# Kernel tuning notes

Measured on AMD Instinct MI355X. Metric: run time of the kernel, lower is better.

## Reference

```python
import jax, jax.numpy as jnp
import numpy as np

DIM = 1024
N_HEADS = 16
HEAD_DIM = DIM // N_HEADS  # 64
FF_DIM = 4096
BATCH = 2
SEQ = 2048
EPS = 1e-8
ROPE_BASE = 10000.0


def _rope_cos_sin(seq_len, head_dim):
    # inv_freq: [head_dim//2]
    inv_freq = 1.0 / (ROPE_BASE ** (jnp.arange(0, head_dim, 2, dtype=jnp.float32) / head_dim))
    t = jnp.arange(seq_len, dtype=jnp.float32)
    freqs = jnp.einsum('i,j->ij', t, inv_freq)          # [S, D/2]
    emb = jnp.concatenate([freqs, freqs], axis=-1)       # [S, D]
    return jnp.cos(emb), jnp.sin(emb)


def _apply_rope(x, cos, sin):
    # x: [B, S, H, D]; cos/sin: [S, D] -> broadcast [1, S, 1, D]
    d2 = x.shape[-1] // 2
    x1, x2 = x[..., :d2], x[..., d2:]
    cos = cos[None, :, None, :]
    sin = sin[None, :, None, :]
    cos1, cos2 = cos[..., :d2], cos[..., d2:]
    sin1, sin2 = sin[..., :d2], sin[..., d2:]
    return jnp.concatenate([x1 * cos1 - x2 * sin1, x1 * sin2 + x2 * cos2], axis=-1)


def _rmsnorm(x, scale):
    # norm = ||x||_2 * d^{-1/2}; out = scale * x / (norm + eps)
    norm = jnp.sqrt(jnp.sum(x * x, axis=-1, keepdims=True)) * (x.shape[-1] ** -0.5)
    return scale * x / (norm + EPS)


def setup_inputs() -> dict:
    key = jax.random.key(0)
    ks = jax.random.split(key, 10)
    s = lambda fan_in: 1.0 / np.sqrt(fan_in)
    return {
        'x': jax.random.normal(ks[0], (BATCH, SEQ, DIM), dtype=jnp.float32),
        'w_qkv': jax.random.normal(ks[1], (DIM, 3 * DIM), dtype=jnp.float32) * s(DIM),
        'w_attn_out': jax.random.normal(ks[2], (DIM, DIM), dtype=jnp.float32) * s(DIM),
        'w_gate': jax.random.normal(ks[3], (DIM, FF_DIM), dtype=jnp.float32) * s(DIM),
        'b_gate': jax.random.normal(ks[4], (FF_DIM,), dtype=jnp.float32) * 0.01,
        'w_lin': jax.random.normal(ks[5], (DIM, FF_DIM), dtype=jnp.float32) * s(DIM),
        'b_lin': jax.random.normal(ks[6], (FF_DIM,), dtype=jnp.float32) * 0.01,
        'w_ff_out': jax.random.normal(ks[7], (FF_DIM, DIM), dtype=jnp.float32) * s(FF_DIM),
        'scale1': jnp.ones((DIM,), dtype=jnp.float32),
        'scale2': jnp.ones((DIM,), dtype=jnp.float32),
    }


def reference(x, w_qkv, w_attn_out, w_gate, b_gate, w_lin, b_lin, w_ff_out, scale1, scale2):
    B, S, _ = x.shape
    residual = x
    qkv = (x @ w_qkv).reshape(B, S, 3, N_HEADS, HEAD_DIM)
    q, k, v = qkv[:, :, 0], qkv[:, :, 1], qkv[:, :, 2]  # [B, S, H, D]
    cos, sin = _rope_cos_sin(S, HEAD_DIM)
    q = _apply_rope(q, cos, sin)
    k = _apply_rope(k, cos, sin)
    # attention scores [B, H, S, S]
    attn = jnp.einsum('bqhd,bkhd->bhqk', q, k) / np.sqrt(HEAD_DIM).astype(np.float32)
    attn = jax.nn.softmax(attn, axis=-1)
    out = jnp.einsum('bhqk,bkhd->bqhd', attn, v).reshape(B, S, DIM)
    out = out @ w_attn_out
    x = _rmsnorm(residual + out, scale1)
    residual = x
    ff = jax.nn.sigmoid(x @ w_gate + b_gate) * (x @ w_lin + b_lin)
    ff = ff @ w_ff_out
    x = _rmsnorm(residual + ff, scale2)
    return x
```

## Files before the change

### kernel.cpp

```cpp
#include <hip/hip_runtime.h>
#include <stdint.h>

#define DIMN 1024
#define NH 16
#define HD 64
#define FFN 4096
#define BBATCH 2
#define SSEQ 2048
#define MROWS (BBATCH*SSEQ)

typedef __bf16 bf16;
typedef __bf16 bf16x8 __attribute__((ext_vector_type(8)));
typedef __bf16 bf16x4 __attribute__((ext_vector_type(4)));
typedef float f32x4 __attribute__((ext_vector_type(4)));
typedef float f32x16 __attribute__((ext_vector_type(16)));
typedef uint32_t u32x4 __attribute__((ext_vector_type(4)));

#define AS1 __attribute__((address_space(1)))
#define AS3 __attribute__((address_space(3)))

__device__ __forceinline__ void gload16(const bf16* g, bf16* l) {
  __builtin_amdgcn_global_load_lds((AS1 const void*)g, (AS3 void*)l, 16, 0, 0);
}

__device__ __forceinline__ uint32_t pkbf(float a, float b) {
  union { bf16 h[2]; uint32_t u; } x;
  x.h[0] = (bf16)a; x.h[1] = (bf16)b;
  return x.u;
}

__global__ void rope_table_kernel(float* __restrict__ tab) {
  int i = blockIdx.x * blockDim.x + threadIdx.x;
  int s = i >> 5, d = i & 31;
  float invf = exp2f(-(float)d * 0.4152410118609203f);
  float fr = (float)s * invf;
  tab[s*64 + d]      = cosf(fr);
  tab[s*64 + 32 + d] = sinf(fr);
}

__global__ void cast_f32_bf16(const float* __restrict__ in, bf16* __restrict__ out, int n4) {
  int i = blockIdx.x * blockDim.x + threadIdx.x;
  if (i < n4) {
    f32x4 v = ((const f32x4*)in)[i];
    bf16x4 o = {(bf16)v.x, (bf16)v.y, (bf16)v.z, (bf16)v.w};
    ((bf16x4*)out)[i] = o;
  }
}

__global__ __launch_bounds__(256) void transpose_cast_f32_bf16(
    const float* __restrict__ in, bf16* __restrict__ out, int R, int C) {
  __shared__ float t[32][33];
  int bx = blockIdx.x, by = blockIdx.y;
  int x = threadIdx.x, y = threadIdx.y;
  #pragma unroll
  for (int j = 0; j < 4; ++j) {
    int r = by*32 + y*4 + j;
    t[y*4+j][x] = in[(size_t)r*C + bx*32 + x];
  }
  __syncthreads();
  #pragma unroll
  for (int j = 0; j < 4; ++j) {
    int c = bx*32 + y*4 + j;
    out[(size_t)c*R + by*32 + x] = (bf16)t[x][y*4+j];
  }
}

template<int NP>
__global__ __launch_bounds__(256) void rmsnorm_sum_kernel(
    const float* __restrict__ parts, const float* __restrict__ resid,
    const float* __restrict__ sc,
    float* __restrict__ outf, bf16* __restrict__ outb) {
  int row = blockIdx.x;
  int tid = threadIdx.x;
  size_t off = (size_t)row * DIMN;
  f32x4 v = ((const f32x4*)(resid + off))[tid];
  #pragma unroll
  for (int p = 0; p < NP; ++p) {
    f32x4 a = ((const f32x4*)(parts + (size_t)p * MROWS * DIMN + off))[tid];
    v.x += a.x; v.y += a.y; v.z += a.z; v.w += a.w;
  }
  float ss = v.x*v.x + v.y*v.y + v.z*v.z + v.w*v.w;
  #pragma unroll
  for (int m = 1; m < 64; m <<= 1) ss += __shfl_xor(ss, m);
  __shared__ float red[4];
  if ((tid & 63) == 0) red[tid >> 6] = ss;
  __syncthreads();
  float tot = red[0] + red[1] + red[2] + red[3];
  float inv = 1.f / (sqrtf(tot) * 0.03125f + 1e-8f);
  f32x4 s4 = ((const f32x4*)sc)[tid];
  f32x4 o = {v.x*s4.x*inv, v.y*s4.y*inv, v.z*s4.z*inv, v.w*s4.w*inv};
  if (outf) ((f32x4*)(outf + off))[tid] = o;
  if (outb) {
    bf16x4 ob = {(bf16)o.x, (bf16)o.y, (bf16)o.z, (bf16)o.w};
    ((bf16x4*)(outb + off))[tid] = ob;
  }
}

template<int EPI>
__global__ void __launch_bounds__(256, 2) gemm_bt(
    const bf16* __restrict__ A, const bf16* __restrict__ B,
    int M, int N, int K,
    void* __restrict__ o0, void* __restrict__ o1, void* __restrict__ o2,
    const void* __restrict__ a0, const void* __restrict__ a1) {
  constexpr bool FUSED = (EPI == 5);
  __shared__ __align__(16) bf16 sh_a[2*4096];
  __shared__ __align__(16) bf16 sh_b[2*4096];
  __shared__ __align__(16) bf16 sh_c[FUSED ? 2*4096 : 4];
  const int tid  = threadIdx.x;
  const int lane = tid & 63;
  const int wid  = tid >> 6;

  int gx  = gridDim.x;
  int bid = blockIdx.y * gx + blockIdx.x;
  int nwg = gx * gridDim.y;
  int cpx = nwg >> 3;
  int swz = (bid & 7) * cpx + (bid >> 3);
  int bxi = swz % gx, byi = swz / gx;

  const int m0 = byi * 128, n0 = bxi * 128;
  const int wm = (wid >> 1) * 64, wn = (wid & 1) * 64;

  const int kb = blockIdx.z;
  const int KC = K / (int)gridDim.z;

  f32x4 acc[4][4] = {};
  f32x4 acc2[FUSED ? 4 : 1][FUSED ? 4 : 1] = {};

  const bf16* a_base = A + (size_t)m0 * K + (size_t)kb * KC;
  const bf16* b_base = B + (size_t)n0 * K + (size_t)kb * KC;
  const bf16* c_base = nullptr;
  if constexpr (FUSED) c_base = (const bf16*)o1 + (size_t)n0 * K;

  auto stage = [&](int kt, int buf) {
    const int lb = buf * 4096;
    #pragma unroll
    for (int i = 0; i < 2; ++i) {
      int idx = i*256 + tid;
      size_t go = (size_t)(idx >> 2)*K + (size_t)kt*32 + (idx & 3)*8;
      gload16(a_base + go, &sh_a[lb + idx*8]);
    }
    #pragma unroll
    for (int i = 0; i < 2; ++i) {
      int idx = i*256 + tid;
      size_t go = (size_t)(idx >> 2)*K + (size_t)kt*32 + (idx & 3)*8;
      gload16(b_base + go, &sh_b[lb + idx*8]);
    }
    if constexpr (FUSED) {
      #pragma unroll
      for (int i = 0; i < 2; ++i) {
        int idx = i*256 + tid;
        size_t go = (size_t)(idx >> 2)*K + (size_t)kt*32 + (idx & 3)*8;
        gload16(c_base + go, &sh_c[lb + idx*8]);
      }
    }
  };

  const int nsteps = KC >> 5;
  stage(0, 0);
  for (int t = 0; t < nsteps; ++t) {
    const int cb = t & 1;
    if (t + 1 < nsteps) {
      stage(t+1, cb ^ 1);
      if constexpr (FUSED) asm volatile("s_waitcnt vmcnt(6)" ::: "memory");
      else                 asm volatile("s_waitcnt vmcnt(4)" ::: "memory");
    } else {
      asm volatile("s_waitcnt vmcnt(0)" ::: "memory");
    }
    __builtin_amdgcn_sched_barrier(0);
    __builtin_amdgcn_s_barrier();
    __builtin_amdgcn_sched_barrier(0);

    const int lb = cb * 4096;
    bf16x8 af[4], bfr[4];
    #pragma unroll
    for (int m = 0; m < 4; ++m)
      af[m] = *(const bf16x8*)&sh_a[lb + (wm + m*16 + (lane & 15))*32 + (lane >> 4)*8];
    #pragma unroll
    for (int n = 0; n < 4; ++n)
      bfr[n] = *(const bf16x8*)&sh_b[lb + (wn + n*16 + (lane & 15))*32 + (lane >> 4)*8];
    __builtin_amdgcn_s_setprio(1);
    #pragma unroll
    for (int m = 0; m < 4; ++m)
      #pragma unroll
      for (int n = 0; n < 4; ++n)
        acc[m][n] = __builtin_amdgcn_mfma_f32_16x16x32_bf16(af[m], bfr[n], acc[m][n], 0, 0, 0);
    __builtin_amdgcn_s_setprio(0);
    if constexpr (FUSED) {
      bf16x8 cf[4];
      #pragma unroll
      for (int n = 0; n < 4; ++n)
        cf[n] = *(const bf16x8*)&sh_c[lb + (wn + n*16 + (lane & 15))*32 + (lane >> 4)*8];
      __builtin_amdgcn_s_setprio(1);
      #pragma unroll
      for (int m = 0; m < 4; ++m)
        #pragma unroll
        for (int n = 0; n < 4; ++n)
          acc2[m][n] = __builtin_amdgcn_mfma_f32_16x16x32_bf16(af[m], cf[n], acc2[m][n], 0, 0, 0);
      __builtin_amdgcn_s_setprio(0);
    }
    __builtin_amdgcn_sched_barrier(0);
    __builtin_amdgcn_s_barrier();
  }

  const int rq = (lane >> 4) * 4;
  const int cl = lane & 15;

  if constexpr (EPI == 0) {
    bf16* q_p = (bf16*)o0; bf16* k_p = (bf16*)o1; bf16* v_p = (bf16*)o2;
    const float* rope = (const float*)a0;
    int sec = (n0 + wn) >> 10;
    int h   = ((n0 + wn) & 1023) >> 6;
    const float qsc = (sec == 0) ? 0.18033688011112042f : 1.0f;
    #pragma unroll
    for (int m = 0; m < 4; ++m) {
      #pragma unroll
      for (int reg = 0; reg < 4; ++reg) {
        int r  = m0 + wm + m*16 + rq + reg;
        int b_ = r >> 11, s_ = r & 2047;
        int tile = s_ >> 5;
        size_t tb = ((size_t)(b_*NH + h) * 64 + tile) * 2048;
        if (sec == 2) {
          int kvl = s_ & 31;
          int ks = kvl >> 4, hiv = (kvl >> 3) & 1, jv = kvl & 7;
          #pragma unroll
          for (int n = 0; n < 4; ++n) {
            int half = n >> 1;
            int qlv  = (n & 1) * 16 + cl;
            v_p[tb + (size_t)(ks*2 + half)*512 + (hiv*32 + qlv)*8 + jv] =
                (bf16)acc[m][n][reg];
          }
        } else {
          int qlt = s_ & 31;
          bf16* dst = (sec == 0 ? q_p : k_p);
          int lo = ((cl >> 3) * 32 + qlt) * 8 + (cl & 7);
          #pragma unroll
          for (int n = 0; n < 2; ++n) {
            int d1 = n*16 + cl;
            float c1 = rope[s_*64 + d1];
            float s1 = rope[s_*64 + 32 + d1];
            float x1 = acc[m][n][reg], x2 = acc[m][n+2][reg];
            dst[tb + (size_t)n*512 + lo]       = (bf16)((x1*c1 - x2*s1) * qsc);
            dst[tb + (size_t)(n+2)*512 + lo]   = (bf16)((x1*s1 + x2*c1) * qsc);
          }
        }
      }
    }
  } else if constexpr (EPI == 1) {
    float* op = (float*)o0;
    const float* rp = (const float*)a0;
    #pragma unroll
    for (int m = 0; m < 4; ++m)
      #pragma unroll
      for (int n = 0; n < 4; ++n)
        #pragma unroll
        for (int reg = 0; reg < 4; ++reg) {
          int r = m0 + wm + m*16 + rq + reg;
          int c = n0 + wn + n*16 + cl;
          op[(size_t)r*N + c] = acc[m][n][reg] + rp[(size_t)r*N + c];
        }
  } else if constexpr (EPI == 4) {
    float* op = (float*)o0 + (size_t)kb * M * N;
    #pragma unroll
    for (int m = 0; m < 4; ++m)
      #pragma unroll
      for (int n = 0; n < 4; ++n)
        #pragma unroll
        for (int reg = 0; reg < 4; ++reg) {
          int r = m0 + wm + m*16 + rq + reg;
          int c = n0 + wn + n*16 + cl;
          op[(size_t)r*N + c] = acc[m][n][reg];
        }
  } else if constexpr (EPI == 5) {
    bf16* op = (bf16*)o0;
    const float* bg = (const float*)a0;
    const float* bl = (const float*)a1;
    #pragma unroll
    for (int m = 0; m < 4; ++m)
      #pragma unroll
      for (int n = 0; n < 4; ++n)
        #pragma unroll
        for (int reg = 0; reg < 4; ++reg) {
          int r = m0 + wm + m*16 + rq + reg;
          int c = n0 + wn + n*16 + cl;
          float gv = acc[m][n][reg] + bg[c];
          float lv = acc2[m][n][reg] + bl[c];
          float s  = 1.f / (1.f + __expf(-gv));
          op[(size_t)r*N + c] = (bf16)(s * lv);
        }
  }
}

__global__ void __launch_bounds__(256) attn_kernel(
    const bf16* __restrict__ qf_g, const bf16* __restrict__ kf_g,
    const bf16* __restrict__ vf_g, bf16* __restrict__ ao_g) {
  __shared__ __align__(16) bf16 lds_k[2*2048];
  __shared__ __align__(16) bf16 lds_v[2*2048];
  const int tid  = threadIdx.x;
  const int lane = tid & 63;
  const int qw   = tid >> 6;
  const int hi   = lane >> 5;
  const int ql   = lane & 31;
  const int bh   = blockIdx.y;
  const int b_   = bh >> 4, h = bh & 15;
  const int q0   = blockIdx.x * 128 + qw * 32;
  const int qt   = blockIdx.x * 4 + qw;

  const bf16* qtile = qf_g + ((size_t)bh*64 + qt) * 2048;
  const bf16* kbase = kf_g + (size_t)bh * 64 * 2048;
  const bf16* vbase = vf_g + (size_t)bh * 64 * 2048;

  bf16x8 qf[4];
  #pragma unroll
  for (int ds = 0; ds < 4; ++ds)
    qf[ds] = *(const bf16x8*)&qtile[ds*512 + lane*8];

  f32x16 o0 = {}, o1 = {};
  float lrun = 0.f;

  gload16(kbase + tid*8, &lds_k[tid*8]);
  gload16(vbase + tid*8, &lds_v[tid*8]);

  for (int t = 0; t < 64; ++t) {
    const int cur = (t & 1) * 2048;
    if (t < 63) {
      const int nxt = 2048 - cur;
      gload16(kbase + (size_t)(t+1)*2048 + tid*8, &lds_k[nxt + tid*8]);
      gload16(vbase + (size_t)(t+1)*2048 + tid*8, &lds_v[nxt + tid*8]);
      asm volatile("s_waitcnt vmcnt(2)" ::: "memory");
    } else {
      asm volatile("s_waitcnt vmcnt(0)" ::: "memory");
    }
    __builtin_amdgcn_sched_barrier(0);
    __builtin_amdgcn_s_barrier();
    __builtin_amdgcn_sched_barrier(0);

    f32x16 st = {};
    __builtin_amdgcn_s_setprio(1);
    #pragma unroll
    for (int ds = 0; ds < 4; ++ds) {
      bf16x8 kf = *(const bf16x8*)&lds_k[cur + ds*512 + lane*8];
      st = __builtin_amdgcn_mfma_f32_32x32x16_bf16(kf, qf[ds], st, 0, 0, 0);
    }
    __builtin_amdgcn_s_setprio(0);
    float p[16];
    float psum = 0.f;
    #pragma unroll
    for (int r = 0; r < 16; ++r) { p[r] = __builtin_amdgcn_exp2f(st[r]); psum += p[r]; }
    lrun += psum;

    uint32_t w0 = pkbf(p[0],p[1]),   w1 = pkbf(p[2],p[3]);
    uint32_t w2 = pkbf(p[4],p[5]),   w3 = pkbf(p[6],p[7]);
    uint32_t w4 = pkbf(p[8],p[9]),   w5 = pkbf(p[10],p[11]);
    uint32_t w6 = pkbf(p[12],p[13]), w7 = pkbf(p[14],p[15]);
    asm("v_permlane32_swap_b32 %0, %1" : "+v"(w0), "+v"(w2));
    asm("v_permlane32_swap_b32 %0, %1" : "+v"(w1), "+v"(w3));
    asm("v_permlane32_swap_b32 %0, %1" : "+v"(w4), "+v"(w6));
    asm("v_permlane32_swap_b32 %0, %1" : "+v"(w5), "+v"(w7));

    __builtin_amdgcn_s_setprio(1);
    {
      union { u32x4 u; bf16x8 b; } pu;
      u32x4 pwa = {w0, w1, w2, w3};
      pu.u = pwa;
      bf16x8 v0 = *(const bf16x8*)&lds_v[cur + 0*512 + lane*8];
      bf16x8 v1 = *(const bf16x8*)&lds_v[cur + 1*512 + lane*8];
      o0 = __builtin_amdgcn_mfma_f32_32x32x16_bf16(v0, pu.b, o0, 0, 0, 0);
      o1 = __builtin_amdgcn_mfma_f32_32x32x16_bf16(v1, pu.b, o1, 0, 0, 0);
      u32x4 pwb = {w4, w5, w6, w7};
      pu.u = pwb;
      bf16x8 v2 = *(const bf16x8*)&lds_v[cur + 2*512 + lane*8];
      bf16x8 v3 = *(const bf16x8*)&lds_v[cur + 3*512 + lane*8];
      o0 = __builtin_amdgcn_mfma_f32_32x32x16_bf16(v2, pu.b, o0, 0, 0, 0);
      o1 = __builtin_amdgcn_mfma_f32_32x32x16_bf16(v3, pu.b, o1, 0, 0, 0);
    }
    __builtin_amdgcn_s_setprio(0);

    __builtin_amdgcn_sched_barrier(0);
    __builtin_amdgcn_s_barrier();
    __builtin_amdgcn_sched_barrier(0);
  }

  lrun += __shfl_xor(lrun, 32);
  float inv = 1.f / lrun;
  bf16* aop = ao_g + ((size_t)(b_*SSEQ) + q0 + ql) * DIMN + h*HD;
  #pragma unroll
  for (int g = 0; g < 4; ++g) {
    int dbase = 8*g + 4*hi;
    bf16x4 w0 = {(bf16)(o0[4*g]*inv), (bf16)(o0[4*g+1]*inv),
                 (bf16)(o0[4*g+2]*inv), (bf16)(o0[4*g+3]*inv)};
    *(bf16x4*)&aop[dbase] = w0;
    bf16x4 w1 = {(bf16)(o1[4*g]*inv), (bf16)(o1[4*g+1]*inv),
                 (bf16)(o1[4*g+2]*inv), (bf16)(o1[4*g+3]*inv)};
    *(bf16x4*)&aop[32 + dbase] = w1;
  }
}

extern "C" void kernel_launch(void* const* d_in, const int* in_sizes, int n_in,
                              void* d_out, int out_size, void* d_ws, size_t ws_size,
                              hipStream_t stream) {
  const float* x      = (const float*)d_in[0];
  const float* w_qkv  = (const float*)d_in[1];
  const float* w_ao   = (const float*)d_in[2];
  const float* w_gate = (const float*)d_in[3];
  const float* b_gate = (const float*)d_in[4];
  const float* w_lin  = (const float*)d_in[5];
  const float* b_lin  = (const float*)d_in[6];
  const float* w_ffo  = (const float*)d_in[7];
  const float* scale1 = (const float*)d_in[8];
  const float* scale2 = (const float*)d_in[9];
  float* out = (float*)d_out;
  (void)ws_size; (void)in_sizes; (void)n_in; (void)out_size;

  uint8_t* ws = (uint8_t*)d_ws;
  bf16*  wt_ws   = (bf16*) (ws + 0);
  float* rope_ws = (float*)(ws + 8388608);
  bf16*  xb_ws   = (bf16*) (ws + 8912896);
  bf16*  ao_ws   = (bf16*) (ws + 8912896);
  bf16*  q_ws    = (bf16*) (ws + 17301504);
  bf16*  k_ws    = (bf16*) (ws + 25690112);
  bf16*  v_ws    = (bf16*) (ws + 34078720);
  float* p1_ws   = (float*)(ws + 17301504);
  bf16*  wt2_ws  = (bf16*) (ws + 50855936);
  bf16*  h1b_ws  = (bf16*) (ws + 84410368);
  bf16*  ffb_ws  = (bf16*) (ws + 8912896);
  float* p2_ws   = (float*)(ws + 42467328);
  float* h1f_ws  = (float*)(ws + 109576192);

  rope_table_kernel<<<256, 256, 0, stream>>>(rope_ws);
  cast_f32_bf16<<<4096, 256, 0, stream>>>(x, xb_ws, MROWS*DIMN/4);
  transpose_cast_f32_bf16<<<dim3(3*DIMN/32, DIMN/32), dim3(32,8), 0, stream>>>(w_qkv, wt_ws, DIMN, 3*DIMN);
  gemm_bt<0><<<dim3(24, 32), 256, 0, stream>>>(xb_ws, wt_ws, MROWS, 3*DIMN, DIMN,
                                               q_ws, k_ws, v_ws, rope_ws, nullptr);
  attn_kernel<<<dim3(16, 32), 256, 0, stream>>>(q_ws, k_ws, v_ws, ao_ws);
  transpose_cast_f32_bf16<<<dim3(DIMN/32, DIMN/32), dim3(32,8), 0, stream>>>(w_ao, wt_ws, DIMN, DIMN);
  gemm_bt<4><<<dim3(8, 32, 2), 256, 0, stream>>>(ao_ws, wt_ws, MROWS, DIMN, DIMN,
                                                 p1_ws, nullptr, nullptr, nullptr, nullptr);
  rmsnorm_sum_kernel<2><<<MROWS, 256, 0, stream>>>(p1_ws, x, scale1, h1f_ws, h1b_ws);
  transpose_cast_f32_bf16<<<dim3(FFN/32, DIMN/32), dim3(32,8), 0, stream>>>(w_gate, wt_ws, DIMN, FFN);
  transpose_cast_f32_bf16<<<dim3(FFN/32, DIMN/32), dim3(32,8), 0, stream>>>(w_lin, wt2_ws, DIMN, FFN);
  gemm_bt<5><<<dim3(32, 32), 256, 0, stream>>>(h1b_ws, wt_ws, MROWS, FFN, DIMN,
                                               ffb_ws, wt2_ws, nullptr, b_gate, b_lin);
  transpose_cast_f32_bf16<<<dim3(DIMN/32, FFN/32), dim3(32,8), 0, stream>>>(w_ffo, wt_ws, FFN, DIMN);
  gemm_bt<4><<<dim3(8, 32, 4), 256, 0, stream>>>(ffb_ws, wt_ws, MROWS, DIMN, FFN,
                                                 p2_ws, nullptr, nullptr, nullptr, nullptr);
  rmsnorm_sum_kernel<4><<<MROWS, 256, 0, stream>>>(p2_ws, h1f_ws, scale2, out, nullptr);
}
```

Before: 311.6 us.

## Add 256-row 8-wave GEMM kernel for FFN gate/lin and output projections

```diff
diff --git a/kernel.cpp b/kernel.cpp
--- a/kernel.cpp
+++ b/kernel.cpp
@@ -102,10 +102,8 @@
     int M, int N, int K,
     void* __restrict__ o0, void* __restrict__ o1, void* __restrict__ o2,
     const void* __restrict__ a0, const void* __restrict__ a1) {
-  constexpr bool FUSED = (EPI == 5);
   __shared__ __align__(16) bf16 sh_a[2*4096];
   __shared__ __align__(16) bf16 sh_b[2*4096];
-  __shared__ __align__(16) bf16 sh_c[FUSED ? 2*4096 : 4];
   const int tid  = threadIdx.x;
   const int lane = tid & 63;
   const int wid  = tid >> 6;
@@ -124,12 +122,9 @@
   const int KC = K / (int)gridDim.z;
 
   f32x4 acc[4][4] = {};
-  f32x4 acc2[FUSED ? 4 : 1][FUSED ? 4 : 1] = {};
 
   const bf16* a_base = A + (size_t)m0 * K + (size_t)kb * KC;
   const bf16* b_base = B + (size_t)n0 * K + (size_t)kb * KC;
-  const bf16* c_base = nullptr;
-  if constexpr (FUSED) c_base = (const bf16*)o1 + (size_t)n0 * K;
 
   auto stage = [&](int kt, int buf) {
     const int lb = buf * 4096;
@@ -144,14 +139,6 @@
       int idx = i*256 + tid;
       size_t go = (size_t)(idx >> 2)*K + (size_t)kt*32 + (idx & 3)*8;
       gload16(b_base + go, &sh_b[lb + idx*8]);
-    }
-    if constexpr (FUSED) {
-      #pragma unroll
-      for (int i = 0; i < 2; ++i) {
-        int idx = i*256 + tid;
-        size_t go = (size_t)(idx >> 2)*K + (size_t)kt*32 + (idx & 3)*8;
-        gload16(c_base + go, &sh_c[lb + idx*8]);
-      }
     }
   };
 
@@ -161,8 +148,7 @@
     const int cb = t & 1;
     if (t + 1 < nsteps) {
       stage(t+1, cb ^ 1);
-      if constexpr (FUSED) asm volatile("s_waitcnt vmcnt(6)" ::: "memory");
-      else                 asm volatile("s_waitcnt vmcnt(4)" ::: "memory");
+      asm volatile("s_waitcnt vmcnt(4)" ::: "memory");
     } else {
       asm volatile("s_waitcnt vmcnt(0)" ::: "memory");
     }
@@ -185,19 +171,6 @@
       for (int n = 0; n < 4; ++n)
         acc[m][n] = __builtin_amdgcn_mfma_f32_16x16x32_bf16(af[m], bfr[n], acc[m][n], 0, 0, 0);
     __builtin_amdgcn_s_setprio(0);
-    if constexpr (FUSED) {
-      bf16x8 cf[4];
-      #pragma unroll
-      for (int n = 0; n < 4; ++n)
-        cf[n] = *(const bf16x8*)&sh_c[lb + (wn + n*16 + (lane & 15))*32 + (lane >> 4)*8];
-      __builtin_amdgcn_s_setprio(1);
-      #pragma unroll
-      for (int m = 0; m < 4; ++m)
-        #pragma unroll
-        for (int n = 0; n < 4; ++n)
-          acc2[m][n] = __builtin_amdgcn_mfma_f32_16x16x32_bf16(af[m], cf[n], acc2[m][n], 0, 0, 0);
-      __builtin_amdgcn_s_setprio(0);
-    }
     __builtin_amdgcn_sched_barrier(0);
     __builtin_amdgcn_s_barrier();
   }
@@ -245,19 +218,6 @@
         }
       }
     }
-  } else if constexpr (EPI == 1) {
-    float* op = (float*)o0;
-    const float* rp = (const float*)a0;
-    #pragma unroll
-    for (int m = 0; m < 4; ++m)
-      #pragma unroll
-      for (int n = 0; n < 4; ++n)
-        #pragma unroll
-        for (int reg = 0; reg < 4; ++reg) {
-          int r = m0 + wm + m*16 + rq + reg;
-          int c = n0 + wn + n*16 + cl;
-          op[(size_t)r*N + c] = acc[m][n][reg] + rp[(size_t)r*N + c];
-        }
   } else if constexpr (EPI == 4) {
     float* op = (float*)o0 + (size_t)kb * M * N;
     #pragma unroll
@@ -270,22 +230,163 @@
           int c = n0 + wn + n*16 + cl;
           op[(size_t)r*N + c] = acc[m][n][reg];
         }
+  }
+}
+
+template<int EPI>
+__global__ void __launch_bounds__(512, 2) gemm256(
+    const bf16* __restrict__ A, const bf16* __restrict__ B,
+    int M, int N, int K,
+    void* __restrict__ o0, const void* __restrict__ o1,
+    const void* __restrict__ a0, const void* __restrict__ a1) {
+  constexpr bool FUSED = (EPI == 5);
+  constexpr int BN = FUSED ? 128 : 256;
+  constexpr int NW = FUSED ? 32 : 64;
+  constexpr int NR = FUSED ? 2 : 4;
+  __shared__ __align__(16) bf16 shA[2][256*32];
+  __shared__ __align__(16) bf16 shB[2][BN*32];
+  __shared__ __align__(16) bf16 shC[FUSED ? 2 : 1][FUSED ? 128*32 : 4];
+  const int tid  = threadIdx.x;
+  const int lane = tid & 63;
+  const int wid  = tid >> 6;
+  const int wr   = wid >> 2;
+  const int wc   = wid & 3;
+
+  int gx  = gridDim.x;
+  int bid = blockIdx.y * gx + blockIdx.x;
+  int nwg = gx * gridDim.y;
+  int cpx = nwg >> 3;
+  int swz = (bid & 7) * cpx + (bid >> 3);
+  int bxi = swz % gx, byi = swz / gx;
+  const int m0 = byi * 256, n0 = bxi * BN;
+
+  const int kb = blockIdx.z;
+  const int KC = K / (int)gridDim.z;
+  const int nt = KC >> 5;
+
+  const bf16* a_base = A + (size_t)m0 * K + (size_t)kb * KC;
+  const bf16* b_base = B + (size_t)n0 * K + (size_t)kb * KC;
+  const bf16* c_base = FUSED ? ((const bf16*)o1 + (size_t)n0 * K) : nullptr;
+
+  const int srow = tid >> 2;
+  const int scol = (tid & 3) * 8;
+  auto stA = [&](int c, int kt, int s) {
+    int row = c*128 + srow;
+    gload16(a_base + (size_t)row*K + kt*32 + scol, &shA[s][row*32 + scol]);
+  };
+  auto stB = [&](int c, int kt, int s) {
+    int row = c*128 + srow;
+    gload16(b_base + (size_t)row*K + kt*32 + scol, &shB[s][row*32 + scol]);
+  };
+  auto stC = [&](int kt, int s) {
+    if constexpr (FUSED)
+      gload16(c_base + (size_t)srow*K + kt*32 + scol, &shC[s][srow*32 + scol]);
+  };
+
+  f32x4 acc [8][NR] = {};
+  f32x4 acc2[FUSED ? 8 : 1][FUSED ? NR : 1] = {};
+
+  stA(0, 0, 0); stA(1, 0, 0);
+  if constexpr (FUSED) { stB(0, 0, 0); stC(0, 0); }
+  else                 { stB(0, 0, 0); stB(1, 0, 0); }
+
+  for (int t = 0; t < nt; ++t) {
+    const int s = t & 1;
+    if (t + 1 < nt) {
+      stA(0, t+1, s^1); stA(1, t+1, s^1);
+      asm volatile("s_waitcnt vmcnt(2)" ::: "memory");
+    } else {
+      asm volatile("s_waitcnt vmcnt(0)" ::: "memory");
+    }
+    __builtin_amdgcn_sched_barrier(0);
+    __builtin_amdgcn_s_barrier();
+    __builtin_amdgcn_sched_barrier(0);
+
+    bf16x8 bfr[NR], cfr[FUSED ? NR : 1];
+    #pragma unroll
+    for (int n = 0; n < NR; ++n)
+      bfr[n] = *(const bf16x8*)&shB[s][(wc*NW + n*16 + (lane & 15))*32 + (lane >> 4)*8];
+    if constexpr (FUSED) {
+      #pragma unroll
+      for (int n = 0; n < NR; ++n)
+        cfr[n] = *(const bf16x8*)&shC[s][(wc*NW + n*16 + (lane & 15))*32 + (lane >> 4)*8];
+    }
+    {
+      bf16x8 af[4];
+      #pragma unroll
+      for (int m = 0; m < 4; ++m)
+        af[m] = *(const bf16x8*)&shA[s][(wr*128 + m*16 + (lane & 15))*32 + (lane >> 4)*8];
+      __builtin_amdgcn_s_setprio(1);
+      #pragma unroll
+      for (int m = 0; m < 4; ++m) {
+        #pragma unroll
+        for (int n = 0; n < NR; ++n) {
+          acc[m][n] = __builtin_amdgcn_mfma_f32_16x16x32_bf16(af[m], bfr[n], acc[m][n], 0, 0, 0);
+          if constexpr (FUSED)
+            acc2[m][n] = __builtin_amdgcn_mfma_f32_16x16x32_bf16(af[m], cfr[n], acc2[m][n], 0, 0, 0);
+        }
+      }
+      __builtin_amdgcn_s_setprio(0);
+    }
+    if (t + 1 < nt) {
+      if constexpr (FUSED) stB(0, t+1, s^1);
+      else                 stB(0, t+1, s^1);
+    }
+    {
+      bf16x8 af[4];
+      #pragma unroll
+      for (int m = 0; m < 4; ++m)
+        af[m] = *(const bf16x8*)&shA[s][(wr*128 + (m+4)*16 + (lane & 15))*32 + (lane >> 4)*8];
+      __builtin_amdgcn_s_setprio(1);
+      #pragma unroll
+      for (int m = 0; m < 4; ++m) {
+        #pragma unroll
+        for (int n = 0; n < NR; ++n) {
+          acc[m+4][n] = __builtin_amdgcn_mfma_f32_16x16x32_bf16(af[m], bfr[n], acc[m+4][n], 0, 0, 0);
+          if constexpr (FUSED)
+            acc2[m+4][n] = __builtin_amdgcn_mfma_f32_16x16x32_bf16(af[m], cfr[n], acc2[m+4][n], 0, 0, 0);
+        }
+      }
+      __builtin_amdgcn_s_setprio(0);
+    }
+    if (t + 1 < nt) {
+      if constexpr (FUSED) stC(t+1, s^1);
+      else                 stB(1, t+1, s^1);
+    }
+    __builtin_amdgcn_sched_barrier(0);
+    __builtin_amdgcn_s_barrier();
+  }
+
+  const int rq = (lane >> 4) * 4;
+  const int cl = lane & 15;
+  if constexpr (EPI == 4) {
+    float* op = (float*)o0 + (size_t)kb * M * N;
+    #pragma unroll
+    for (int m = 0; m < 8; ++m)
+      #pragma unroll
+      for (int n = 0; n < NR; ++n)
+        #pragma unroll
+        for (int reg = 0; reg < 4; ++reg) {
+          int r = m0 + wr*128 + m*16 + rq + reg;
+          int c = n0 + wc*NW + n*16 + cl;
+          op[(size_t)r*N + c] = acc[m][n][reg];
+        }
   } else if constexpr (EPI == 5) {
     bf16* op = (bf16*)o0;
     const float* bg = (const float*)a0;
     const float* bl = (const float*)a1;
     #pragma unroll
-    for (int m = 0; m < 4; ++m)
-      #pragma unroll
-      for (int n = 0; n < 4; ++n)
+    for (int m = 0; m < 8; ++m)
+      #pragma unroll
+      for (int n = 0; n < NR; ++n)
         #pragma unroll
         for (int reg = 0; reg < 4; ++reg) {
-          int r = m0 + wm + m*16 + rq + reg;
-          int c = n0 + wn + n*16 + cl;
-          float gv = acc[m][n][reg] + bg[c];
+          int r = m0 + wr*128 + m*16 + rq + reg;
+          int c = n0 + wc*NW + n*16 + cl;
+          float gv = acc[m][n][reg]  + bg[c];
           float lv = acc2[m][n][reg] + bl[c];
-          float s  = 1.f / (1.f + __expf(-gv));
-          op[(size_t)r*N + c] = (bf16)(s * lv);
+          float sg = 1.f / (1.f + __expf(-gv));
+          op[(size_t)r*N + c] = (bf16)(sg * lv);
         }
   }
 }
@@ -438,10 +539,10 @@
   rmsnorm_sum_kernel<2><<<MROWS, 256, 0, stream>>>(p1_ws, x, scale1, h1f_ws, h1b_ws);
   transpose_cast_f32_bf16<<<dim3(FFN/32, DIMN/32), dim3(32,8), 0, stream>>>(w_gate, wt_ws, DIMN, FFN);
   transpose_cast_f32_bf16<<<dim3(FFN/32, DIMN/32), dim3(32,8), 0, stream>>>(w_lin, wt2_ws, DIMN, FFN);
-  gemm_bt<5><<<dim3(32, 32), 256, 0, stream>>>(h1b_ws, wt_ws, MROWS, FFN, DIMN,
-                                               ffb_ws, wt2_ws, nullptr, b_gate, b_lin);
+  gemm256<5><<<dim3(32, 16), 512, 0, stream>>>(h1b_ws, wt_ws, MROWS, FFN, DIMN,
+                                               ffb_ws, wt2_ws, b_gate, b_lin);
   transpose_cast_f32_bf16<<<dim3(DIMN/32, FFN/32), dim3(32,8), 0, stream>>>(w_ffo, wt_ws, FFN, DIMN);
-  gemm_bt<4><<<dim3(8, 32, 4), 256, 0, stream>>>(ffb_ws, wt_ws, MROWS, DIMN, FFN,
-                                                 p2_ws, nullptr, nullptr, nullptr, nullptr);
+  gemm256<4><<<dim3(4, 16, 4), 512, 0, stream>>>(ffb_ws, wt_ws, MROWS, DIMN, FFN,
+                                                 p2_ws, nullptr, nullptr, nullptr);
   rmsnorm_sum_kernel<4><<<MROWS, 256, 0, stream>>>(p2_ws, h1f_ws, scale2, out, nullptr);
 }
```

Result: slower. 328.0 us (+5.3%).

## Add dedicated 256x128 fused gate/lin GEMM kernel with 4-stage A pipeline

Applied to the files above, without the earlier changes.

```diff
diff --git a/kernel.cpp b/kernel.cpp
--- a/kernel.cpp
+++ b/kernel.cpp
@@ -102,10 +102,8 @@
     int M, int N, int K,
     void* __restrict__ o0, void* __restrict__ o1, void* __restrict__ o2,
     const void* __restrict__ a0, const void* __restrict__ a1) {
-  constexpr bool FUSED = (EPI == 5);
   __shared__ __align__(16) bf16 sh_a[2*4096];
   __shared__ __align__(16) bf16 sh_b[2*4096];
-  __shared__ __align__(16) bf16 sh_c[FUSED ? 2*4096 : 4];
   const int tid  = threadIdx.x;
   const int lane = tid & 63;
   const int wid  = tid >> 6;
@@ -124,12 +122,9 @@
   const int KC = K / (int)gridDim.z;
 
   f32x4 acc[4][4] = {};
-  f32x4 acc2[FUSED ? 4 : 1][FUSED ? 4 : 1] = {};
 
   const bf16* a_base = A + (size_t)m0 * K + (size_t)kb * KC;
   const bf16* b_base = B + (size_t)n0 * K + (size_t)kb * KC;
-  const bf16* c_base = nullptr;
-  if constexpr (FUSED) c_base = (const bf16*)o1 + (size_t)n0 * K;
 
   auto stage = [&](int kt, int buf) {
     const int lb = buf * 4096;
@@ -144,14 +139,6 @@
       int idx = i*256 + tid;
       size_t go = (size_t)(idx >> 2)*K + (size_t)kt*32 + (idx & 3)*8;
       gload16(b_base + go, &sh_b[lb + idx*8]);
-    }
-    if constexpr (FUSED) {
-      #pragma unroll
-      for (int i = 0; i < 2; ++i) {
-        int idx = i*256 + tid;
-        size_t go = (size_t)(idx >> 2)*K + (size_t)kt*32 + (idx & 3)*8;
-        gload16(c_base + go, &sh_c[lb + idx*8]);
-      }
     }
   };
 
@@ -161,8 +148,7 @@
     const int cb = t & 1;
     if (t + 1 < nsteps) {
       stage(t+1, cb ^ 1);
-      if constexpr (FUSED) asm volatile("s_waitcnt vmcnt(6)" ::: "memory");
-      else                 asm volatile("s_waitcnt vmcnt(4)" ::: "memory");
+      asm volatile("s_waitcnt vmcnt(4)" ::: "memory");
     } else {
       asm volatile("s_waitcnt vmcnt(0)" ::: "memory");
     }
@@ -185,19 +171,6 @@
       for (int n = 0; n < 4; ++n)
         acc[m][n] = __builtin_amdgcn_mfma_f32_16x16x32_bf16(af[m], bfr[n], acc[m][n], 0, 0, 0);
     __builtin_amdgcn_s_setprio(0);
-    if constexpr (FUSED) {
-      bf16x8 cf[4];
-      #pragma unroll
-      for (int n = 0; n < 4; ++n)
-        cf[n] = *(const bf16x8*)&sh_c[lb + (wn + n*16 + (lane & 15))*32 + (lane >> 4)*8];
-      __builtin_amdgcn_s_setprio(1);
-      #pragma unroll
-      for (int m = 0; m < 4; ++m)
-        #pragma unroll
-        for (int n = 0; n < 4; ++n)
-          acc2[m][n] = __builtin_amdgcn_mfma_f32_16x16x32_bf16(af[m], cf[n], acc2[m][n], 0, 0, 0);
-      __builtin_amdgcn_s_setprio(0);
-    }
     __builtin_amdgcn_sched_barrier(0);
     __builtin_amdgcn_s_barrier();
   }
@@ -245,19 +218,6 @@
         }
       }
     }
-  } else if constexpr (EPI == 1) {
-    float* op = (float*)o0;
-    const float* rp = (const float*)a0;
-    #pragma unroll
-    for (int m = 0; m < 4; ++m)
-      #pragma unroll
-      for (int n = 0; n < 4; ++n)
-        #pragma unroll
-        for (int reg = 0; reg < 4; ++reg) {
-          int r = m0 + wm + m*16 + rq + reg;
-          int c = n0 + wn + n*16 + cl;
-          op[(size_t)r*N + c] = acc[m][n][reg] + rp[(size_t)r*N + c];
-        }
   } else if constexpr (EPI == 4) {
     float* op = (float*)o0 + (size_t)kb * M * N;
     #pragma unroll
@@ -270,24 +230,127 @@
           int c = n0 + wn + n*16 + cl;
           op[(size_t)r*N + c] = acc[m][n][reg];
         }
-  } else if constexpr (EPI == 5) {
-    bf16* op = (bf16*)o0;
-    const float* bg = (const float*)a0;
-    const float* bl = (const float*)a1;
-    #pragma unroll
-    for (int m = 0; m < 4; ++m)
-      #pragma unroll
-      for (int n = 0; n < 4; ++n)
+  }
+}
+
+__global__ void __launch_bounds__(512, 2) gemm256_ffn1(
+    const bf16* __restrict__ A, const bf16* __restrict__ Bg,
+    const bf16* __restrict__ Bl, int M, int N, int K,
+    bf16* __restrict__ o0, const float* __restrict__ bgv,
+    const float* __restrict__ blv) {
+  __shared__ __align__(16) bf16 shA[4][256*32];
+  const int tid  = threadIdx.x;
+  const int lane = tid & 63;
+  const int wid  = tid >> 6;
+  const int wr   = wid >> 2;
+  const int wc   = wid & 3;
+
+  int gx  = gridDim.x;
+  int bid = blockIdx.y * gx + blockIdx.x;
+  int nwg = gx * gridDim.y;
+  int cpx = nwg >> 3;
+  int swz = (bid & 7) * cpx + (bid >> 3);
+  int bxi = swz % gx, byi = swz / gx;
+  const int m0 = byi * 256, n0 = bxi * 128;
+
+  const int nt = K >> 5;
+
+  const bf16* a_base  = A  + (size_t)m0 * K;
+  const bf16* bg_base = Bg + (size_t)(n0 + wc*32) * K;
+  const bf16* bl_base = Bl + (size_t)(n0 + wc*32) * K;
+
+  const int fr = lane & 15, fq = lane >> 4;
+
+  const int srow = tid >> 2;
+  const int snom = tid & 3;
+  const int sgl  = snom ^ (srow & 3);
+  auto stA = [&](int kt, int s) {
+    #pragma unroll
+    for (int c = 0; c < 2; ++c) {
+      int row = c*128 + srow;
+      gload16(a_base + (size_t)row*K + (size_t)kt*32 + sgl*8,
+              &shA[s][row*32 + snom*8]);
+    }
+  };
+  auto ldBC = [&](int kt, bf16x8* bb, bf16x8* cc) {
+    #pragma unroll
+    for (int n = 0; n < 2; ++n) {
+      bb[n] = *(const bf16x8*)(bg_base + (size_t)(n*16 + fr)*K + (size_t)kt*32 + fq*8);
+      cc[n] = *(const bf16x8*)(bl_base + (size_t)(n*16 + fr)*K + (size_t)kt*32 + fq*8);
+    }
+  };
+
+  f32x4 acc [8][2] = {};
+  f32x4 acc2[8][2] = {};
+  bf16x8 bcur[2], ccur[2], bnxt[2], cnxt[2];
+
+  stA(0, 0); stA(1, 1); stA(2, 2);
+  ldBC(0, bcur, ccur);
+
+  const int aslot = (fq ^ (fr & 3)) * 8;
+
+  for (int t = 0; t < nt; ++t) {
+    const int s = t & 3;
+    if (t + 3 < nt) stA(t+3, (t+3) & 3);
+    if (t + 1 < nt) ldBC(t+1, bnxt, cnxt);
+    if (t + 3 < nt)      asm volatile("s_waitcnt vmcnt(10)" ::: "memory");
+    else if (t + 1 < nt) asm volatile("s_waitcnt vmcnt(8)" ::: "memory");
+    else                 asm volatile("s_waitcnt vmcnt(0)" ::: "memory");
+    __builtin_amdgcn_sched_barrier(0);
+    __builtin_amdgcn_s_barrier();
+    __builtin_amdgcn_sched_barrier(0);
+
+    {
+      bf16x8 af[4];
+      #pragma unroll
+      for (int m = 0; m < 4; ++m)
+        af[m] = *(const bf16x8*)&shA[s][(wr*128 + m*16 + fr)*32 + aslot];
+      __builtin_amdgcn_s_setprio(1);
+      #pragma unroll
+      for (int m = 0; m < 4; ++m)
         #pragma unroll
-        for (int reg = 0; reg < 4; ++reg) {
-          int r = m0 + wm + m*16 + rq + reg;
-          int c = n0 + wn + n*16 + cl;
-          float gv = acc[m][n][reg] + bg[c];
-          float lv = acc2[m][n][reg] + bl[c];
-          float s  = 1.f / (1.f + __expf(-gv));
-          op[(size_t)r*N + c] = (bf16)(s * lv);
+        for (int n = 0; n < 2; ++n) {
+          acc [m][n] = __builtin_amdgcn_mfma_f32_16x16x32_bf16(af[m], bcur[n], acc [m][n], 0, 0, 0);
+          acc2[m][n] = __builtin_amdgcn_mfma_f32_16x16x32_bf16(af[m], ccur[n], acc2[m][n], 0, 0, 0);
         }
-  }
+      __builtin_amdgcn_s_setprio(0);
+    }
+    {
+      bf16x8 af[4];
+      #pragma unroll
+      for (int m = 0; m < 4; ++m)
+        af[m] = *(const bf16x8*)&shA[s][(wr*128 + (m+4)*16 + fr)*32 + aslot];
+      __builtin_amdgcn_s_setprio(1);
+      #pragma unroll
+      for (int m = 0; m < 4; ++m)
+        #pragma unroll
+        for (int n = 0; n < 2; ++n) {
+          acc [m+4][n] = __builtin_amdgcn_mfma_f32_16x16x32_bf16(af[m], bcur[n], acc [m+4][n], 0, 0, 0);
+          acc2[m+4][n] = __builtin_amdgcn_mfma_f32_16x16x32_bf16(af[m], ccur[n], acc2[m+4][n], 0, 0, 0);
+        }
+      __builtin_amdgcn_s_setprio(0);
+    }
+    __builtin_amdgcn_sched_barrier(0);
+    __builtin_amdgcn_s_barrier();
+    #pragma unroll
+    for (int n = 0; n < 2; ++n) { bcur[n] = bnxt[n]; ccur[n] = cnxt[n]; }
+  }
+
+  const int rq = (lane >> 4) * 4;
+  const int cl = lane & 15;
+  #pragma unroll
+  for (int m = 0; m < 8; ++m)
+    #pragma unroll
+    for (int n = 0; n < 2; ++n)
+      #pragma unroll
+      for (int reg = 0; reg < 4; ++reg) {
+        int r = m0 + wr*128 + m*16 + rq + reg;
+        int c = n0 + wc*32 + n*16 + cl;
+        float gv = acc [m][n][reg] + bgv[c];
+        float lv = acc2[m][n][reg] + blv[c];
+        float sg = 1.f / (1.f + __expf(-gv));
+        o0[(size_t)r*N + c] = (bf16)(sg * lv);
+      }
 }
 
 __global__ void __launch_bounds__(256) attn_kernel(
@@ -438,8 +501,8 @@
   rmsnorm_sum_kernel<2><<<MROWS, 256, 0, stream>>>(p1_ws, x, scale1, h1f_ws, h1b_ws);
   transpose_cast_f32_bf16<<<dim3(FFN/32, DIMN/32), dim3(32,8), 0, stream>>>(w_gate, wt_ws, DIMN, FFN);
   transpose_cast_f32_bf16<<<dim3(FFN/32, DIMN/32), dim3(32,8), 0, stream>>>(w_lin, wt2_ws, DIMN, FFN);
-  gemm_bt<5><<<dim3(32, 32), 256, 0, stream>>>(h1b_ws, wt_ws, MROWS, FFN, DIMN,
-                                               ffb_ws, wt2_ws, nullptr, b_gate, b_lin);
+  gemm256_ffn1<<<dim3(32, 16), 512, 0, stream>>>(h1b_ws, wt_ws, wt2_ws, MROWS, FFN, DIMN,
+                                                 ffb_ws, b_gate, b_lin);
   transpose_cast_f32_bf16<<<dim3(DIMN/32, FFN/32), dim3(32,8), 0, stream>>>(w_ffo, wt_ws, FFN, DIMN);
   gemm_bt<4><<<dim3(8, 32, 4), 256, 0, stream>>>(ffb_ws, wt_ws, MROWS, DIMN, FFN,
                                                  p2_ws, nullptr, nullptr, nullptr, nullptr);
```

Measured after the change: 348.6 us. +11.9%, slower.
